# Kernel optimization log

Measured on AMD Instinct MI355X. Metric: run time of the kernel, lower is better.

## Reference

```python
import jax, jax.numpy as jnp
import numpy as np

D = 2048; H = 8; HD = 256; KV = 4; GHD = 512; GKV = 4; ROT = 128
F = 8192; V = 32000; B = 2; S = 1024; WIN = 512; EPS = 1e-6
THETA_S = 10000.0; THETA_G = 1000000.0


def _rms(x, w):
    return x * jax.lax.rsqrt(jnp.mean(x * x, axis=-1, keepdims=True) + EPS) * w


def _rms_ns(x):
    return x * jax.lax.rsqrt(jnp.mean(x * x, axis=-1, keepdims=True) + EPS)


def _angles(d, theta):
    # cos/sin tables: [S, d//2]
    inv = 1.0 / (theta ** (jnp.arange(0, d, 2, dtype=jnp.float32) / d))
    ang = jnp.arange(S, dtype=jnp.float32)[:, None] * inv[None, :]
    return jnp.cos(ang), jnp.sin(ang)


def _rope(x, cos, sin):
    # x: [B,S,H,d]; interleaved complex rotation on pairs
    b, s, h, d = x.shape
    xr = x.reshape(b, s, h, d // 2, 2)
    x1, x2 = xr[..., 0], xr[..., 1]
    c = cos[None, :, None, :]
    sn = sin[None, :, None, :]
    return jnp.stack([x1 * c - x2 * sn, x1 * sn + x2 * c], axis=-1).reshape(b, s, h, d)


def _partial_rope(x, cos, sin, rot):
    if rot == x.shape[-1]:
        return _rope(x, cos, sin)
    return jnp.concatenate([_rope(x[..., :rot], cos, sin), x[..., rot:]], axis=-1)


def _block(x, wq, wk, wv, wo, qn, kn, wg, wu, wd, ln1, ln2, ln3, ln4, scal,
           cos, sin, rot, mask, n_rep):
    res = x
    h = _rms(x, ln1)
    xq = jnp.einsum('bsd,dhc->bshc', h, wq)
    xk = jnp.einsum('bsd,dkc->bskc', h, wk)
    if wv is None:
        xv = _rms_ns(xk)  # global block: V = unscaled-RMS-normed K (pre k_norm)
    else:
        xv = _rms_ns(jnp.einsum('bsd,dkc->bskc', h, wv))
    xq = _rms(xq, qn)
    xk = _rms(xk, kn)
    xq = _partial_rope(xq, cos, sin, rot)
    xk = _partial_rope(xk, cos, sin, rot)
    q = xq.transpose(0, 2, 1, 3)  # [B,H,S,d]
    k = xk.transpose(0, 2, 1, 3)
    v = xv.transpose(0, 2, 1, 3)
    if n_rep != 1:
        k = jnp.repeat(k, n_rep, axis=1)
        v = jnp.repeat(v, n_rep, axis=1)
    scores = jnp.einsum('bhqd,bhkd->bhqk', q, k)  # NOTE: no 1/sqrt(d), as in source
    p = jax.nn.softmax(scores.astype(jnp.float32), axis=-1, where=mask[:, None, :, :]).astype(x.dtype)
    o = jnp.einsum('bhqk,bhkd->bhqd', p, v).transpose(0, 2, 1, 3)
    o = o.reshape(x.shape[0], x.shape[1], -1)
    o = _rms(jnp.einsum('bsd,do->bso', o, wo), ln2)
    x = res + o
    res = x
    hf = _rms(x, ln3)
    ffn = jnp.einsum('bsf,fd->bsd',
                     jax.nn.gelu(jnp.einsum('bsd,df->bsf', hf, wg), approximate=True)
                     * jnp.einsum('bsd,df->bsf', hf, wu), wd)
    x = res + _rms(ffn, ln4)
    return x * scal


def setup_inputs() -> dict:
    key = jax.random.key(0)
    ks = jax.random.split(key, 20)
    n = lambda k, shp: jax.random.normal(k, shp, jnp.float32) * 0.02
    inp = {
        'tokens': jax.random.randint(ks[0], (B, S), 0, V, jnp.int32),
        'true_lengths': jnp.full((B,), S, jnp.int32),
        'embed': n(ks[1], (V, D)),
        'norm_w': jnp.ones((D,), jnp.float32),
        's_wq': n(ks[2], (D, H, HD)), 's_wk': n(ks[3], (D, KV, HD)), 's_wv': n(ks[4], (D, KV, HD)),
        's_wo': n(ks[5], (H * HD, D)),
        's_qn': jnp.ones((HD,), jnp.float32), 's_kn': jnp.ones((HD,), jnp.float32),
        's_wg': n(ks[6], (D, F)), 's_wu': n(ks[7], (D, F)), 's_wd': n(ks[8], (F, D)),
        's_ln1': jnp.ones((D,), jnp.float32), 's_ln2': jnp.ones((D,), jnp.float32),
        's_ln3': jnp.ones((D,), jnp.float32), 's_ln4': jnp.ones((D,), jnp.float32),
        's_scal': jnp.ones((1,), jnp.float32),
        'g_wq': n(ks[9], (D, H, GHD)), 'g_wk': n(ks[10], (D, GKV, GHD)),
        'g_wo': n(ks[11], (H * GHD, D)),
        'g_qn': jnp.ones((GHD,), jnp.float32), 'g_kn': jnp.ones((GHD,), jnp.float32),
        'g_wg': n(ks[12], (D, F)), 'g_wu': n(ks[13], (D, F)), 'g_wd': n(ks[14], (F, D)),
        'g_ln1': jnp.ones((D,), jnp.float32), 'g_ln2': jnp.ones((D,), jnp.float32),
        'g_ln3': jnp.ones((D,), jnp.float32), 'g_ln4': jnp.ones((D,), jnp.float32),
        'g_scal': jnp.ones((1,), jnp.float32),
    }
    return inp


def reference(tokens, true_lengths, embed, norm_w,
              s_wq, s_wk, s_wv, s_wo, s_qn, s_kn, s_wg, s_wu, s_wd,
              s_ln1, s_ln2, s_ln3, s_ln4, s_scal,
              g_wq, g_wk, g_wo, g_qn, g_kn, g_wg, g_wu, g_wd,
              g_ln1, g_ln2, g_ln3, g_ln4, g_scal):
    # prefill from empty cache: seq_positions = 0, cache len == seqlen
    qpos = jnp.arange(S)[:, None]
    kpos = jnp.arange(S)[None, :]
    causal = qpos >= kpos
    sw = causal & ((qpos - kpos) < WIN)
    kvalid = kpos[None, 0, :][None, :] if False else (jnp.arange(S)[None, :] < true_lengths[:, None])  # [B,S]
    sliding_mask = sw[None, :, :] & kvalid[:, None, :]
    global_mask = causal[None, :, :] & kvalid[:, None, :]

    cos_s, sin_s = _angles(HD, THETA_S)
    cos_g, sin_g = _angles(ROT, THETA_G)

    h = embed[tokens] * jnp.sqrt(jnp.float32(D))
    h = _block(h, s_wq, s_wk, s_wv, s_wo, s_qn, s_kn, s_wg, s_wu, s_wd,
               s_ln1, s_ln2, s_ln3, s_ln4, s_scal, cos_s, sin_s, HD, sliding_mask, H // KV)
    h = _block(h, g_wq, g_wk, None, g_wo, g_qn, g_kn, g_wg, g_wu, g_wd,
               g_ln1, g_ln2, g_ln3, g_ln4, g_scal, cos_g, sin_g, ROT, global_mask, H // GKV)
    h = _rms(h, norm_w)
    logits = jnp.einsum('bsd,vd->bsv', h, embed)  # tied embedding head
    return logits
```

## Files before the change

kernel.cpp:

```cpp
#include <hip/hip_runtime.h>
#include <math.h>

typedef unsigned short u16;
typedef _Float16 f16;
typedef __attribute__((ext_vector_type(8))) _Float16 f16x8;
typedef __attribute__((ext_vector_type(4))) float f32x4;

constexpr int cB   = 2;
constexpr int cS   = 1024;
constexpr int cD   = 2048;
constexpr int cH   = 8;
constexpr int cHD  = 256;
constexpr int cKV  = 4;
constexpr int cGHD = 512;
constexpr int cGKV = 4;
constexpr int cROT = 128;
constexpr int cF   = 8192;
constexpr int cV   = 32000;
constexpr int cWIN = 512;
constexpr int cM   = cB * cS;
constexpr float cEPS = 1e-6f;
constexpr size_t MB = 1024 * 1024;

__device__ inline u16 f2h(float x) { union { f16 h; u16 u; } c; c.h = (f16)x; return c.u; }
__device__ inline float h2f(u16 v) { union { u16 u; f16 h; } c; c.u = v; return (float)c.h; }

__device__ inline int swz16(int row, int chunk) {
    return row * 32 + ((chunk ^ ((row >> 1) & 3)) << 3);
}
__device__ inline int swzK(int row, int ch) {
    return row * 64 + ((ch ^ (row & 7)) << 3);
}

typedef __attribute__((address_space(1))) const unsigned int gu32;
typedef __attribute__((address_space(3))) unsigned int lu32;
__device__ inline void ldsload16(const u16* g, u16* l) {
    __builtin_amdgcn_global_load_lds((gu32*)g, (lu32*)l, 16, 0, 0);
}

__device__ inline float gelu_tanh(float v) {
    const float t = tanhf(0.7978845608028654f * (v + 0.044715f * v * v * v));
    return 0.5f * v * (1.f + t);
}

__global__ void embed_kernel(const int* __restrict__ tok,
                             const float* __restrict__ emb,
                             float* __restrict__ out) {
    const int row = blockIdx.x;
    const int t = tok[row];
    const float* e = emb + (size_t)t * cD;
    float* o = out + (size_t)row * cD;
    const float sc = sqrtf((float)cD);
    for (int d = threadIdx.x; d < cD; d += blockDim.x) o[d] = e[d] * sc;
}

__global__ void rms_kernel(const float* __restrict__ x,
                           const float* __restrict__ w,
                           float* __restrict__ out, int dim) {
    const int row = blockIdx.x;
    const float* xr = x + (size_t)row * dim;
    float* orow = out + (size_t)row * dim;
    float ss = 0.f;
    for (int d = threadIdx.x; d < dim; d += blockDim.x) { float v = xr[d]; ss += v * v; }
    for (int o = 32; o >= 1; o >>= 1) ss += __shfl_xor(ss, o);
    __shared__ float rb[8];
    if ((threadIdx.x & 63) == 0) rb[threadIdx.x >> 6] = ss;
    __syncthreads();
    ss = rb[0] + rb[1] + rb[2] + rb[3];
    const float r = rsqrtf(ss / dim + cEPS);
    for (int d = threadIdx.x; d < dim; d += blockDim.x)
        orow[d] = xr[d] * r * (w ? w[d] : 1.f);
}

__global__ void rms_f16_kernel(const float* __restrict__ x,
                               const float* __restrict__ w,
                               u16* __restrict__ out, int dim) {
    const int row = blockIdx.x;
    const float* xr = x + (size_t)row * dim;
    u16* orow = out + (size_t)row * dim;
    float ss = 0.f;
    for (int d = threadIdx.x; d < dim; d += blockDim.x) { float v = xr[d]; ss += v * v; }
    for (int o = 32; o >= 1; o >>= 1) ss += __shfl_xor(ss, o);
    __shared__ float rb[8];
    if ((threadIdx.x & 63) == 0) rb[threadIdx.x >> 6] = ss;
    __syncthreads();
    ss = rb[0] + rb[1] + rb[2] + rb[3];
    const float r = rsqrtf(ss / dim + cEPS);
    for (int d = threadIdx.x; d < dim; d += blockDim.x)
        orow[d] = f2h(xr[d] * r * (w ? w[d] : 1.f));
}

__global__ __launch_bounds__(256) void addnorm_kernel(const float* __restrict__ res,
                                                      const float* __restrict__ y,
                                                      const float* __restrict__ w_add,
                                                      const float* __restrict__ scal,
                                                      const float* __restrict__ w_norm,
                                                      float* __restrict__ xout,
                                                      u16* __restrict__ abo) {
    const int row = blockIdx.x;
    const float* yr = y + (size_t)row * cD;
    const float* rr = res + (size_t)row * cD;
    float* xo = xout + (size_t)row * cD;
    u16* ao = abo + (size_t)row * cD;
    const int tid = threadIdx.x;
    __shared__ float rb[4];

    float yl[8], xl[8];
    float ss = 0.f;
#pragma unroll
    for (int j = 0; j < 8; ++j) { yl[j] = yr[tid + j * 256]; ss += yl[j] * yl[j]; }
    for (int o = 32; o >= 1; o >>= 1) ss += __shfl_xor(ss, o);
    if ((tid & 63) == 0) rb[tid >> 6] = ss;
    __syncthreads();
    ss = rb[0] + rb[1] + rb[2] + rb[3];
    const float r1 = rsqrtf(ss / cD + cEPS);
    const float sc = scal ? *scal : 1.f;

    float ss2 = 0.f;
#pragma unroll
    for (int j = 0; j < 8; ++j) {
        const int d = tid + j * 256;
        xl[j] = (rr[d] + yl[j] * r1 * w_add[d]) * sc;
        ss2 += xl[j] * xl[j];
    }
    for (int o = 32; o >= 1; o >>= 1) ss2 += __shfl_xor(ss2, o);
    __syncthreads();
    if ((tid & 63) == 0) rb[tid >> 6] = ss2;
    __syncthreads();
    ss2 = rb[0] + rb[1] + rb[2] + rb[3];
    const float r2 = rsqrtf(ss2 / cD + cEPS);
#pragma unroll
    for (int j = 0; j < 8; ++j) {
        const int d = tid + j * 256;
        xo[d] = xl[j];
        ao[d] = f2h(xl[j] * r2 * w_norm[d]);
    }
}

__global__ __launch_bounds__(128) void rmsrope_kernel(const float* __restrict__ x,
                                                      const float* __restrict__ w,
                                                      u16* __restrict__ out,
                                                      int NH, int HDIM, int rot,
                                                      float theta) {
    const int row = blockIdx.x;
    const int s = (row / NH) % cS;
    const float* xr = x + (size_t)row * HDIM;
    u16* orow = out + (size_t)row * HDIM;
    const int tid = threadIdx.x;
    const int np = HDIM >> 1;
    __shared__ float rb[2];

    float v1[2], v2[2];
    float ss = 0.f;
    for (int p = tid, j = 0; p < np; p += 128, ++j) {
        v1[j] = xr[2 * p]; v2[j] = xr[2 * p + 1];
        ss += v1[j] * v1[j] + v2[j] * v2[j];
    }
    for (int o = 32; o >= 1; o >>= 1) ss += __shfl_xor(ss, o);
    if ((tid & 63) == 0) rb[tid >> 6] = ss;
    __syncthreads();
    ss = rb[0] + rb[1];
    const float r = rsqrtf(ss / HDIM + cEPS);
    const int halfrot = rot >> 1;
    for (int p = tid, j = 0; p < np; p += 128, ++j) {
        const float a = v1[j] * r * w[2 * p];
        const float b = v2[j] * r * w[2 * p + 1];
        float o1 = a, o2 = b;
        if (p < halfrot) {
            const float inv = powf(theta, -(2.f * p) / (float)rot);
            const float ang = (float)s * inv;
            const float c = cosf(ang), sn = sinf(ang);
            o1 = a * c - b * sn;
            o2 = a * sn + b * c;
        }
        orow[2 * p]     = f2h(o1);
        orow[2 * p + 1] = f2h(o2);
    }
}

__global__ __launch_bounds__(256) void tcast_kernel(const float* __restrict__ in,
                                                    u16* __restrict__ out,
                                                    int K, int N, int ldin) {
    __shared__ float t[32][33];
    const int kt = blockIdx.y * 32, nt = blockIdx.x * 32;
    const int tx = threadIdx.x & 31, ty = threadIdx.x >> 5;
#pragma unroll
    for (int j = 0; j < 4; ++j)
        t[ty + j * 8][tx] = in[(size_t)(kt + ty + j * 8) * ldin + nt + tx];
    __syncthreads();
#pragma unroll
    for (int j = 0; j < 4; ++j)
        out[(size_t)(nt + ty + j * 8) * K + kt + tx] = f2h(t[tx][ty + j * 8]);
}

__global__ void cast_f16_kernel(const float* __restrict__ in, u16* __restrict__ out,
                                int n) {
    const int i = blockIdx.x * blockDim.x + threadIdx.x;
    if (i * 4 >= n) return;
    const float4 v = *(const float4*)&in[(size_t)i * 4];
    uint2 o;
    o.x = (unsigned)f2h(v.x) | ((unsigned)f2h(v.y) << 16);
    o.y = (unsigned)f2h(v.z) | ((unsigned)f2h(v.w) << 16);
    *(uint2*)&out[(size_t)i * 4] = o;
}

__global__ __launch_bounds__(256) void vtrans_kernel(const float* __restrict__ V,
                                                     u16* __restrict__ Vt,
                                                     int HDIM, int KVH) {
    __shared__ float t[32][33];
    const int bk = blockIdx.z;
    const int b = bk / KVH, kh = bk % KVH;
    const int st = blockIdx.y * 32, dt = blockIdx.x * 32;
    const int tx = threadIdx.x & 31, ty = threadIdx.x >> 5;
#pragma unroll
    for (int j = 0; j < 4; ++j)
        t[ty + j * 8][tx] = V[((size_t)(b * cS + st + ty + j * 8) * KVH + kh) * HDIM + dt + tx];
    __syncthreads();
#pragma unroll
    for (int j = 0; j < 4; ++j)
        Vt[((size_t)bk * HDIM + dt + ty + j * 8) * cS + st + tx] = f2h(t[tx][ty + j * 8]);
}

template<bool F16_OUT, bool GELU>
__global__ __launch_bounds__(256) void gemm_f16(const u16* __restrict__ A,
                                                const u16* __restrict__ Bt,
                                                void* __restrict__ Cout,
                                                const u16* __restrict__ gate,
                                                int Mt, int K, int ldc) {
    __shared__ u16 As[128 * 32];
    __shared__ u16 Bs[128 * 32];
    const int nwg = gridDim.x;
    const int q8 = nwg >> 3;
    const int dd = blockIdx.x;
    const int wk = (dd & 7) * q8 + (dd >> 3);
    const int bm = (wk % Mt) * 128;
    const int bn = (wk / Mt) * 128;
    const int tid = threadIdx.x;
    const int lane = tid & 63;
    const int wv = tid >> 6;
    const int wr = (wv >> 1) * 64, wc = (wv & 1) * 64;
    const int r15 = lane & 15, hi16 = lane >> 4;

    f32x4 acc[4][4];
#pragma unroll
    for (int m = 0; m < 4; ++m)
#pragma unroll
        for (int n = 0; n < 4; ++n) acc[m][n] = (f32x4){0.f, 0.f, 0.f, 0.f};

    int rowS[2], koS[2];
#pragma unroll
    for (int i = 0; i < 2; ++i) {
        const int s = i * 256 + tid;
        rowS[i] = s >> 2;
        koS[i] = ((s & 3) ^ ((rowS[i] >> 1) & 3)) * 8;
    }
    u16* ldsA0 = &As[(wv * 64) * 8];
    u16* ldsA1 = &As[(256 + wv * 64) * 8];
    u16* ldsB0 = &Bs[(wv * 64) * 8];
    u16* ldsB1 = &Bs[(256 + wv * 64) * 8];

    for (int k0 = 0; k0 < K; k0 += 32) {
        __syncthreads();
        ldsload16(&A [(size_t)(bm + rowS[0]) * K + k0 + koS[0]], ldsA0);
        ldsload16(&A [(size_t)(bm + rowS[1]) * K + k0 + koS[1]], ldsA1);
        ldsload16(&Bt[(size_t)(bn + rowS[0]) * K + k0 + koS[0]], ldsB0);
        ldsload16(&Bt[(size_t)(bn + rowS[1]) * K + k0 + koS[1]], ldsB1);
        __syncthreads();
        f16x8 af[4], bf4[4];
#pragma unroll
        for (int m = 0; m < 4; ++m)
            af[m] = *(const f16x8*)&As[swz16(wr + m * 16 + r15, hi16)];
#pragma unroll
        for (int n = 0; n < 4; ++n)
            bf4[n] = *(const f16x8*)&Bs[swz16(wc + n * 16 + r15, hi16)];
#pragma unroll
        for (int m = 0; m < 4; ++m)
#pragma unroll
            for (int n = 0; n < 4; ++n)
                acc[m][n] = __builtin_amdgcn_mfma_f32_16x16x32_f16(af[m], bf4[n], acc[m][n], 0, 0, 0);
    }
#pragma unroll
    for (int m = 0; m < 4; ++m)
#pragma unroll
        for (int n = 0; n < 4; ++n)
#pragma unroll
            for (int r = 0; r < 4; ++r) {
                const int row = bm + wr + m * 16 + hi16 * 4 + r;
                const int col = bn + wc + n * 16 + r15;
                const size_t idx = (size_t)row * ldc + col;
                float v = acc[m][n][r];
                if (GELU) v = gelu_tanh(h2f(gate[idx])) * v;
                if (F16_OUT) ((u16*)Cout)[idx] = f2h(v);
                else         ((float*)Cout)[idx] = v;
            }
}

__global__ __launch_bounds__(256) void qk_f16(const u16* __restrict__ Qh,
                                              const u16* __restrict__ Kh,
                                              float* __restrict__ Sc,
                                              int HDIM, int KVH, int win) {
    const int bm = blockIdx.y * 128;
    const int bn = blockIdx.x * 128;
    if (bn > bm + 127) return;
    if (win > 0 && bm - bn > win + 126) return;
    const int bh = blockIdx.z;
    const int b = bh / cH, h = bh % cH;
    const int kh = h / (cH / KVH);

    __shared__ u16 As[128 * 64];
    __shared__ u16 Bs[128 * 64];
    const int tid = threadIdx.x;
    const int lane = tid & 63;
    const int w = tid >> 6;
    const int wr = (w >> 1) * 64, wc = (w & 1) * 64;
    const int r15 = lane & 15, hi16 = lane >> 4;

    const int lda = cH * HDIM, ldb = KVH * HDIM;
    const u16* Aq = Qh + ((size_t)b * cS * cH + h) * HDIM;
    const u16* Bk = Kh + ((size_t)b * cS * KVH + kh) * HDIM;

    f32x4 acc[4][4];
#pragma unroll
    for (int m = 0; m < 4; ++m)
#pragma unroll
        for (int n = 0; n < 4; ++n) acc[m][n] = (f32x4){0.f, 0.f, 0.f, 0.f};

    int rA[4], cA[4], wl[4];
#pragma unroll
    for (int j = 0; j < 4; ++j) {
        const int c = tid + j * 256;
        rA[j] = c >> 3; cA[j] = (c & 7) * 8;
        wl[j] = swzK(rA[j], c & 7);
    }

    for (int k0 = 0; k0 < HDIM; k0 += 64) {
        uint4 av[4], bv[4];
#pragma unroll
        for (int j = 0; j < 4; ++j) {
            av[j] = *(const uint4*)&Aq[(size_t)(bm + rA[j]) * lda + k0 + cA[j]];
            bv[j] = *(const uint4*)&Bk[(size_t)(bn + rA[j]) * ldb + k0 + cA[j]];
        }
        __syncthreads();
#pragma unroll
        for (int j = 0; j < 4; ++j) {
            *(uint4*)&As[wl[j]] = av[j];
            *(uint4*)&Bs[wl[j]] = bv[j];
        }
        __syncthreads();
#pragma unroll
        for (int kk = 0; kk < 2; ++kk) {
            f16x8 af[4], bf4[4];
#pragma unroll
            for (int m = 0; m < 4; ++m)
                af[m] = *(const f16x8*)&As[swzK(wr + m * 16 + r15, kk * 4 + hi16)];
#pragma unroll
            for (int n = 0; n < 4; ++n)
                bf4[n] = *(const f16x8*)&Bs[swzK(wc + n * 16 + r15, kk * 4 + hi16)];
#pragma unroll
            for (int m = 0; m < 4; ++m)
#pragma unroll
                for (int n = 0; n < 4; ++n)
                    acc[m][n] = __builtin_amdgcn_mfma_f32_16x16x32_f16(af[m], bf4[n], acc[m][n], 0, 0, 0);
        }
    }
    float* Crow = Sc + (size_t)bh * cS * cS;
#pragma unroll
    for (int m = 0; m < 4; ++m)
#pragma unroll
        for (int n = 0; n < 4; ++n)
#pragma unroll
            for (int r = 0; r < 4; ++r)
                Crow[(size_t)(bm + wr + m * 16 + hi16 * 4 + r) * cS + bn + wc + n * 16 + r15]
                    = acc[m][n][r];
}

__global__ __launch_bounds__(256) void softmax_kernel(float* __restrict__ Sc,
                                                      const int* __restrict__ tlen,
                                                      int win) {
    const int q = blockIdx.x, bh = blockIdx.y, b = bh / cH;
    float* row = Sc + ((size_t)bh * cS + q) * cS;
    u16* rowh = (u16*)row;
    const int tid = threadIdx.x;
    const int tl = tlen[b];
    const int kmax = min(q, tl - 1);
    const int kmin = (win > 0) ? max(0, q - win + 1) : 0;

    float v[4];
    float m = -1e30f;
#pragma unroll
    for (int j = 0; j < 4; ++j) {
        const int k = tid + j * 256;
        const bool ok = (k >= kmin && k <= kmax);
        v[j] = ok ? row[k] : -1e30f;
        m = fmaxf(m, v[j]);
    }
    for (int o = 32; o >= 1; o >>= 1) m = fmaxf(m, __shfl_xor(m, o));
    __shared__ float rb[8];
    if ((tid & 63) == 0) rb[tid >> 6] = m;
    __syncthreads();
    m = fmaxf(fmaxf(rb[0], rb[1]), fmaxf(rb[2], rb[3]));

    float e[4];
    float s = 0.f;
#pragma unroll
    for (int j = 0; j < 4; ++j) {
        const int k = tid + j * 256;
        const bool ok = (k >= kmin && k <= kmax);
        e[j] = ok ? expf(v[j] - m) : 0.f;
        s += e[j];
    }
    for (int o = 32; o >= 1; o >>= 1) s += __shfl_xor(s, o);
    __shared__ float sb[4];
    if ((tid & 63) == 0) sb[tid >> 6] = s;
    __syncthreads();
    s = sb[0] + sb[1] + sb[2] + sb[3];
    const float inv = 1.f / s;
    __syncthreads();
#pragma unroll
    for (int j = 0; j < 4; ++j) {
        const int k = tid + j * 256;
        rowh[k] = f2h(e[j] * inv);
    }
}

__global__ __launch_bounds__(256) void pv_f16(const u16* __restrict__ P,
                                              const u16* __restrict__ Vt,
                                              u16* __restrict__ O,
                                              int HDIM, int KVH, int win) {
    const int bh = blockIdx.z;
    const int b = bh / cH, h = bh % cH;
    const int kh = h / (cH / KVH);
    const int bm = blockIdx.y * 128;
    const int bn = blockIdx.x * 128;

    __shared__ u16 As[128 * 64];
    __shared__ u16 Bs[128 * 64];
    const int tid = threadIdx.x;
    const int lane = tid & 63;
    const int w = tid >> 6;
    const int wr = (w >> 1) * 64, wc = (w & 1) * 64;
    const int r15 = lane & 15, hi16 = lane >> 4;

    const u16* Ap = P + (size_t)bh * cS * 2048;
    const u16* Bv = Vt + ((size_t)b * KVH + kh) * HDIM * cS;

    f32x4 acc[4][4];
#pragma unroll
    for (int m = 0; m < 4; ++m)
#pragma unroll
        for (int n = 0; n < 4; ++n) acc[m][n] = (f32x4){0.f, 0.f, 0.f, 0.f};

    int rA[4], cA[4], wl[4];
#pragma unroll
    for (int j = 0; j < 4; ++j) {
        const int c = tid + j * 256;
        rA[j] = c >> 3; cA[j] = (c & 7) * 8;
        wl[j] = swzK(rA[j], c & 7);
    }

    const int klo = (win > 0) ? (max(0, bm - win + 1) & ~63) : 0;
    const int khi = min(bm + 128, cS);

    for (int k0 = klo; k0 < khi; k0 += 64) {
        uint4 av[4], bv[4];
#pragma unroll
        for (int j = 0; j < 4; ++j) {
            av[j] = *(const uint4*)&Ap[(size_t)(bm + rA[j]) * 2048 + k0 + cA[j]];
            bv[j] = *(const uint4*)&Bv[(size_t)(bn + rA[j]) * cS + k0 + cA[j]];
        }
        __syncthreads();
#pragma unroll
        for (int j = 0; j < 4; ++j) {
            *(uint4*)&As[wl[j]] = av[j];
            *(uint4*)&Bs[wl[j]] = bv[j];
        }
        __syncthreads();
#pragma unroll
        for (int kk = 0; kk < 2; ++kk) {
            f16x8 af[4], bf4[4];
#pragma unroll
            for (int m = 0; m < 4; ++m)
                af[m] = *(const f16x8*)&As[swzK(wr + m * 16 + r15, kk * 4 + hi16)];
#pragma unroll
            for (int n = 0; n < 4; ++n)
                bf4[n] = *(const f16x8*)&Bs[swzK(wc + n * 16 + r15, kk * 4 + hi16)];
#pragma unroll
            for (int m = 0; m < 4; ++m)
#pragma unroll
                for (int n = 0; n < 4; ++n)
                    acc[m][n] = __builtin_amdgcn_mfma_f32_16x16x32_f16(af[m], bf4[n], acc[m][n], 0, 0, 0);
        }
    }
    const int ldo = cH * HDIM;
#pragma unroll
    for (int m = 0; m < 4; ++m)
#pragma unroll
        for (int n = 0; n < 4; ++n)
#pragma unroll
            for (int r = 0; r < 4; ++r) {
                const int q = bm + wr + m * 16 + hi16 * 4 + r;
                const int d = bn + wc + n * 16 + r15;
                O[(size_t)(b * cS + q) * ldo + h * HDIM + d] = f2h(acc[m][n][r]);
            }
}

extern "C" void kernel_launch(void* const* d_in, const int* in_sizes, int n_in,
                              void* d_out, int out_size, void* d_ws, size_t ws_size,
                              hipStream_t stream) {
    (void)in_sizes; (void)n_in; (void)out_size; (void)ws_size;
    const int*   tokens = (const int*)  d_in[0];
    const int*   tlen   = (const int*)  d_in[1];
    const float* embed  = (const float*)d_in[2];
    const float* norm_w = (const float*)d_in[3];
    const float* s_wq   = (const float*)d_in[4];
    const float* s_wk   = (const float*)d_in[5];
    const float* s_wv   = (const float*)d_in[6];
    const float* s_wo   = (const float*)d_in[7];
    const float* s_qn   = (const float*)d_in[8];
    const float* s_kn   = (const float*)d_in[9];
    const float* s_wg   = (const float*)d_in[10];
    const float* s_wu   = (const float*)d_in[11];
    const float* s_wd   = (const float*)d_in[12];
    const float* s_ln1  = (const float*)d_in[13];
    const float* s_ln2  = (const float*)d_in[14];
    const float* s_ln3  = (const float*)d_in[15];
    const float* s_ln4  = (const float*)d_in[16];
    const float* s_scal = (const float*)d_in[17];
    const float* g_wq   = (const float*)d_in[18];
    const float* g_wk   = (const float*)d_in[19];
    const float* g_wo   = (const float*)d_in[20];
    const float* g_qn   = (const float*)d_in[21];
    const float* g_kn   = (const float*)d_in[22];
    const float* g_wg   = (const float*)d_in[23];
    const float* g_wu   = (const float*)d_in[24];
    const float* g_wd   = (const float*)d_in[25];
    const float* g_ln1  = (const float*)d_in[26];
    const float* g_ln2  = (const float*)d_in[27];
    const float* g_ln3  = (const float*)d_in[28];
    const float* g_ln4  = (const float*)d_in[29];
    const float* g_scal = (const float*)d_in[30];

    char* w8 = (char*)d_ws;
    float* x   = (float*)(w8);
    u16*   ab  = (u16*)(w8 + 16 * MB);
    u16*   wp  = (u16*)(w8 + 24 * MB);
    u16*   Qb  = (u16*)(w8 + 24 * MB);
    u16*   Ob  = (u16*)(w8 + 24 * MB);
    u16*   embH= (u16*)(w8 + 24 * MB);
    u16*   t0b = (u16*)(w8 + 56 * MB);
    u16*   Kb  = (u16*)(w8 + 58 * MB);
    u16*   Vt  = (u16*)(w8 + 75 * MB);
    float* scores = (float*)(w8 + 84 * MB);
    u16*   Pb  = (u16*)(w8 + 84 * MB);
    float* qf  = (float*)(w8 + 84 * MB);
    u16*   wo2 = (u16*)(w8 + 84 * MB);
    u16*   t1b = (u16*)(w8 + 88 * MB);
    float* kf  = (float*)(w8 + 116 * MB);
    float* r0  = (float*)(w8 + 116 * MB);
    float* fo  = (float*)(w8 + 120 * MB);
    float* vf  = (float*)(w8 + 132 * MB);

    auto tcast = [&](const float* in, u16* outp, int K, int N, int ldin) {
        tcast_kernel<<<dim3(N / 32, K / 32), 256, 0, stream>>>(in, outp, K, N, ldin);
    };
    auto gemmF = [&](const u16* A, const u16* Bt, float* C, int N, int K, int ldc) {
        gemm_f16<false, false><<<16 * (N / 128), 256, 0, stream>>>(A, Bt, C, nullptr, 16, K, ldc);
    };
    auto gemmH = [&](const u16* A, const u16* Bt, u16* C, int N, int K, int ldc) {
        gemm_f16<true, false><<<16 * (N / 128), 256, 0, stream>>>(A, Bt, C, nullptr, 16, K, ldc);
    };
    auto gemmHG = [&](const u16* A, const u16* Bt, u16* C, const u16* gate,
                      int N, int K, int ldc) {
        gemm_f16<true, true><<<16 * (N / 128), 256, 0, stream>>>(A, Bt, C, gate, 16, K, ldc);
    };

    auto attention = [&](int HDIM, int KVH, int win) {
        vtrans_kernel<<<dim3(HDIM / 32, cS / 32, cB * KVH), 256, 0, stream>>>(vf, Vt, HDIM, KVH);
        qk_f16<<<dim3(cS / 128, cS / 128, cB * cH), 256, 0, stream>>>(
            Qb, Kb, scores, HDIM, KVH, win);
        softmax_kernel<<<dim3(cS, cB * cH), 256, 0, stream>>>(scores, tlen, win);
        pv_f16<<<dim3(HDIM / 128, cS / 128, cB * cH), 256, 0, stream>>>(
            Pb, Vt, Ob, HDIM, KVH, win);
    };

    embed_kernel<<<cM, 256, 0, stream>>>(tokens, embed, x);

    rms_f16_kernel<<<cM, 256, 0, stream>>>(x, s_ln1, ab, cD);
    tcast(s_wq, wp, cD, cH * cHD, cH * cHD);
    gemmF(ab, wp, qf, cH * cHD, cD, cH * cHD);
    tcast(s_wk, wp, cD, cKV * cHD, cKV * cHD);
    gemmF(ab, wp, kf, cKV * cHD, cD, cKV * cHD);
    tcast(s_wv, wp, cD, cKV * cHD, cKV * cHD);
    gemmF(ab, wp, vf, cKV * cHD, cD, cKV * cHD);
    rms_kernel<<<cM * cKV, 256, 0, stream>>>(vf, nullptr, vf, cHD);
    rmsrope_kernel<<<cM * cH, 128, 0, stream>>>(qf, s_qn, Qb, cH, cHD, cHD, 10000.f);
    rmsrope_kernel<<<cM * cKV, 128, 0, stream>>>(kf, s_kn, Kb, cKV, cHD, cHD, 10000.f);
    attention(cHD, cKV, cWIN);
    tcast(s_wo, wo2, cH * cHD, cD, cD);
    gemmF(Ob, wo2, r0, cD, cH * cHD, cD);
    addnorm_kernel<<<cM, 256, 0, stream>>>(x, r0, s_ln2, nullptr, s_ln3, x, ab);
    tcast(s_wg, wp, cD, cF, cF);
    gemmH(ab, wp, t1b, cF, cD, cF);
    tcast(s_wu, wp, cD, cF, cF);
    gemmHG(ab, wp, t0b, t1b, cF, cD, cF);
    tcast(s_wd, wp, cF, cD, cD);
    gemmF(t0b, wp, fo, cD, cF, cD);
    addnorm_kernel<<<cM, 256, 0, stream>>>(x, fo, s_ln4, s_scal, g_ln1, x, ab);

    tcast(g_wq, wp, cD, cH * cGHD, cH * cGHD);
    gemmF(ab, wp, qf, cH * cGHD, cD, cH * cGHD);
    tcast(g_wk, wp, cD, cGKV * cGHD, cGKV * cGHD);
    gemmF(ab, wp, kf, cGKV * cGHD, cD, cGKV * cGHD);
    rms_kernel<<<cM * cGKV, 256, 0, stream>>>(kf, nullptr, vf, cGHD);
    rmsrope_kernel<<<cM * cH, 128, 0, stream>>>(qf, g_qn, Qb, cH, cGHD, cROT, 1000000.f);
    rmsrope_kernel<<<cM * cGKV, 128, 0, stream>>>(kf, g_kn, Kb, cGKV, cGHD, cROT, 1000000.f);
    attention(cGHD, cGKV, 0);
    tcast(g_wo, wo2, cH * cGHD, cD, cD);
    gemmF(Ob, wo2, r0, cD, cH * cGHD, cD);
    addnorm_kernel<<<cM, 256, 0, stream>>>(x, r0, g_ln2, nullptr, g_ln3, x, ab);
    tcast(g_wg, wp, cD, cF, cF);
    gemmH(ab, wp, t1b, cF, cD, cF);
    tcast(g_wu, wp, cD, cF, cF);
    gemmHG(ab, wp, t0b, t1b, cF, cD, cF);
    tcast(g_wd, wp, cF, cD, cD);
    gemmF(t0b, wp, fo, cD, cF, cD);
    addnorm_kernel<<<cM, 256, 0, stream>>>(x, fo, g_ln4, g_scal, norm_w, x, ab);

    cast_f16_kernel<<<(cV * cD / 4 + 255) / 256, 256, 0, stream>>>(embed, embH, cV * cD);
    gemm_f16<false, false><<<16 * (cV / 128), 256, 0, stream>>>(
        ab, embH, (float*)d_out, nullptr, 16, cD, cV);
}
```

Baseline: 2.257 ms.

## Add 256x256-tile double-buffered GEMM for FFN gate/up and logits

Adds a 512-thread GEMM kernel that computes 256x256 output tiles, double-buffers its LDS tiles, and remaps workgroups so consecutive tiles are grouped per XCD. The FFN gate and up projections and the tied-embedding logits GEMM now use it instead of the 128x128 kernel. The aim is more operand reuse per byte loaded and better L2 locality on these large GEMMs. The cost is higher register and LDS pressure (128 accumulator floats per thread, 64KB LDS) and fewer workgroups, which lowers occupancy.

```diff
diff --git a/kernel.cpp b/kernel.cpp
--- a/kernel.cpp
+++ b/kernel.cpp
@@ -289,6 +289,100 @@
                 const int col = bn + wc + n * 16 + r15;
                 const size_t idx = (size_t)row * ldc + col;
                 float v = acc[m][n][r];
+                if (GELU) v = gelu_tanh(h2f(gate[idx])) * v;
+                if (F16_OUT) ((u16*)Cout)[idx] = f2h(v);
+                else         ((float*)Cout)[idx] = v;
+            }
+}
+
+template<bool F16_OUT, bool GELU>
+__global__ __launch_bounds__(512) void gemm256(const u16* __restrict__ A,
+                                               const u16* __restrict__ Bt,
+                                               void* __restrict__ Cout,
+                                               const u16* __restrict__ gate,
+                                               int Mt, int K, int ldc) {
+    __shared__ u16 As[2][256 * 32];
+    __shared__ u16 Bs[2][256 * 32];
+    const int nwg = gridDim.x;
+    const int q8 = nwg >> 3;
+    const int dd = blockIdx.x;
+    const int wk = (dd & 7) * q8 + (dd >> 3);
+    const int bm = (wk % Mt) * 256;
+    const int bn = (wk / Mt) * 256;
+    const int tid = threadIdx.x;
+    const int lane = tid & 63;
+    const int wid = tid >> 6;
+    const int wm = wid >> 2, wn = wid & 3;
+    const int r15 = lane & 15, hi16 = lane >> 4;
+
+    f32x4 acc[8][4];
+#pragma unroll
+    for (int mi = 0; mi < 8; ++mi)
+#pragma unroll
+        for (int ni = 0; ni < 4; ++ni) acc[mi][ni] = (f32x4){0.f, 0.f, 0.f, 0.f};
+
+    const int rpl  = lane >> 3;
+    const int ch8d = (lane & 7) ^ rpl;
+    const int sr   = wid * 16 + rpl * 2 + (ch8d >> 2);
+    const int sk   = (ch8d & 3) * 8;
+    const int ldst = wid * 512;
+
+    const int nt = K / 32;
+    {
+        ldsload16(&A [(size_t)(bm + sr)       * K + sk], &As[0][ldst]);
+        ldsload16(&A [(size_t)(bm + 128 + sr) * K + sk], &As[0][4096 + ldst]);
+        ldsload16(&Bt[(size_t)(bn + sr)       * K + sk], &Bs[0][ldst]);
+        ldsload16(&Bt[(size_t)(bn + 128 + sr) * K + sk], &Bs[0][4096 + ldst]);
+    }
+    __syncthreads();
+
+    for (int t = 0; t < nt; ++t) {
+        const int cur = t & 1;
+        if (t + 1 < nt) {
+            const int nb = cur ^ 1;
+            const size_t k0 = (size_t)(t + 1) * 32 + sk;
+            ldsload16(&A [(size_t)(bm + sr)       * K + k0], &As[nb][ldst]);
+            ldsload16(&A [(size_t)(bm + 128 + sr) * K + k0], &As[nb][4096 + ldst]);
+            ldsload16(&Bt[(size_t)(bn + sr)       * K + k0], &Bs[nb][ldst]);
+            ldsload16(&Bt[(size_t)(bn + 128 + sr) * K + k0], &Bs[nb][4096 + ldst]);
+        }
+        const u16* Ab = As[cur];
+        const u16* Bb = Bs[cur];
+        f16x8 bf[4], af[8];
+#pragma unroll
+        for (int ni = 0; ni < 4; ++ni) {
+            const int row = wn * 64 + ni * 16 + r15;
+            const int rp = row >> 1;
+            const int slot = (((row & 1) << 2) | hi16) ^ (rp & 7);
+            bf[ni] = *(const f16x8*)&Bb[rp * 64 + slot * 8];
+        }
+#pragma unroll
+        for (int mi = 0; mi < 8; ++mi) {
+            const int row = wm * 128 + mi * 16 + r15;
+            const int rp = row >> 1;
+            const int slot = (((row & 1) << 2) | hi16) ^ (rp & 7);
+            af[mi] = *(const f16x8*)&Ab[rp * 64 + slot * 8];
+        }
+        __builtin_amdgcn_s_setprio(1);
+#pragma unroll
+        for (int mi = 0; mi < 8; ++mi)
+#pragma unroll
+            for (int ni = 0; ni < 4; ++ni)
+                acc[mi][ni] = __builtin_amdgcn_mfma_f32_16x16x32_f16(af[mi], bf[ni], acc[mi][ni], 0, 0, 0);
+        __builtin_amdgcn_s_setprio(0);
+        __syncthreads();
+    }
+
+#pragma unroll
+    for (int mi = 0; mi < 8; ++mi)
+#pragma unroll
+        for (int ni = 0; ni < 4; ++ni)
+#pragma unroll
+            for (int r = 0; r < 4; ++r) {
+                const int row = bm + wm * 128 + mi * 16 + hi16 * 4 + r;
+                const int col = bn + wn * 64 + ni * 16 + r15;
+                const size_t idx = (size_t)row * ldc + col;
+                float v = acc[mi][ni][r];
                 if (GELU) v = gelu_tanh(h2f(gate[idx])) * v;
                 if (F16_OUT) ((u16*)Cout)[idx] = f2h(v);
                 else         ((float*)Cout)[idx] = v;
@@ -566,12 +660,15 @@
     auto gemmF = [&](const u16* A, const u16* Bt, float* C, int N, int K, int ldc) {
         gemm_f16<false, false><<<16 * (N / 128), 256, 0, stream>>>(A, Bt, C, nullptr, 16, K, ldc);
     };
-    auto gemmH = [&](const u16* A, const u16* Bt, u16* C, int N, int K, int ldc) {
-        gemm_f16<true, false><<<16 * (N / 128), 256, 0, stream>>>(A, Bt, C, nullptr, 16, K, ldc);
+    auto g256F = [&](const u16* A, const u16* Bt, float* C, int N, int K, int ldc) {
+        gemm256<false, false><<<8 * (N / 256), 512, 0, stream>>>(A, Bt, C, nullptr, 8, K, ldc);
     };
-    auto gemmHG = [&](const u16* A, const u16* Bt, u16* C, const u16* gate,
+    auto g256H = [&](const u16* A, const u16* Bt, u16* C, int N, int K, int ldc) {
+        gemm256<true, false><<<8 * (N / 256), 512, 0, stream>>>(A, Bt, C, nullptr, 8, K, ldc);
+    };
+    auto g256HG = [&](const u16* A, const u16* Bt, u16* C, const u16* gate,
                       int N, int K, int ldc) {
-        gemm_f16<true, true><<<16 * (N / 128), 256, 0, stream>>>(A, Bt, C, gate, 16, K, ldc);
+        gemm256<true, true><<<8 * (N / 256), 512, 0, stream>>>(A, Bt, C, gate, 8, K, ldc);
     };
 
     auto attention = [&](int HDIM, int KVH, int win) {
@@ -600,9 +697,9 @@
     gemmF(Ob, wo2, r0, cD, cH * cHD, cD);
     addnorm_kernel<<<cM, 256, 0, stream>>>(x, r0, s_ln2, nullptr, s_ln3, x, ab);
     tcast(s_wg, wp, cD, cF, cF);
-    gemmH(ab, wp, t1b, cF, cD, cF);
+    g256H(ab, wp, t1b, cF, cD, cF);
     tcast(s_wu, wp, cD, cF, cF);
-    gemmHG(ab, wp, t0b, t1b, cF, cD, cF);
+    g256HG(ab, wp, t0b, t1b, cF, cD, cF);
     tcast(s_wd, wp, cF, cD, cD);
     gemmF(t0b, wp, fo, cD, cF, cD);
     addnorm_kernel<<<cM, 256, 0, stream>>>(x, fo, s_ln4, s_scal, g_ln1, x, ab);
@@ -619,14 +716,14 @@
     gemmF(Ob, wo2, r0, cD, cH * cGHD, cD);
     addnorm_kernel<<<cM, 256, 0, stream>>>(x, r0, g_ln2, nullptr, g_ln3, x, ab);
     tcast(g_wg, wp, cD, cF, cF);
-    gemmH(ab, wp, t1b, cF, cD, cF);
+    g256H(ab, wp, t1b, cF, cD, cF);
     tcast(g_wu, wp, cD, cF, cF);
-    gemmHG(ab, wp, t0b, t1b, cF, cD, cF);
+    g256HG(ab, wp, t0b, t1b, cF, cD, cF);
     tcast(g_wd, wp, cF, cD, cD);
     gemmF(t0b, wp, fo, cD, cF, cD);
     addnorm_kernel<<<cM, 256, 0, stream>>>(x, fo, g_ln4, g_scal, norm_w, x, ab);
 
     cast_f16_kernel<<<(cV * cD / 4 + 255) / 256, 256, 0, stream>>>(embed, embH, cV * cD);
-    gemm_f16<false, false><<<16 * (cV / 128), 256, 0, stream>>>(
-        ab, embH, (float*)d_out, nullptr, 16, cD, cV);
-}
+    gemm256<false, false><<<8 * (cV / 256), 512, 0, stream>>>(
+        ab, embH, (float*)d_out, nullptr, 8, cD, cV);
+}
```

Result: faster. 2.056 ms (-8.9%).
